# Kernel tuning notes

Hardware: AMD Instinct MI355X
Metric: run time of the kernel (lower is better)

Reference implementation:

```python
import jax, jax.numpy as jnp
import numpy as np

N_NODES = 10000
N_EDGES = 160000
C = 128           # channel multiplicity
D_DOWN = 64       # node_feats_down '64x0e'
D_RAD = 8         # radial basis size
AVG_NEIGH = 16.0
INV_SQRT3 = 1.0 / np.sqrt(3.0)  # CG coeff for 1o x 1o -> 0e


def setup_inputs() -> dict:
    key = jax.random.key(0)
    ks = jax.random.split(key, 20)
    inp = {
        "node_attrs": jax.random.normal(ks[0], (N_NODES, 10), jnp.float32),
        "node_feats": jax.random.normal(ks[1], (N_NODES, 4 * C), jnp.float32),
        "edge_attrs": jax.random.normal(ks[2], (N_EDGES, 4), jnp.float32),
        "edge_feats": jax.random.uniform(ks[3], (N_EDGES, D_RAD), jnp.float32),
        "edge_index": jax.random.randint(ks[4], (N_EDGES, 2), 0, N_NODES, jnp.int32),
        # linear_up: 128x0e+128x1o -> 128x0e+128x1o (per-irrep channel mixing)
        "W_up0": jax.random.normal(ks[5], (C, C), jnp.float32),
        "W_up1": jax.random.normal(ks[6], (C, C), jnp.float32),
        # linear_down: 128x0e+128x1o -> 64x0e (only scalars map)
        "W_down": jax.random.normal(ks[7], (C, D_DOWN), jnp.float32),
        # radial MLP [136, 256, 256, 256, 512]
        "Wm0": jax.random.normal(ks[8], (D_RAD + 2 * D_DOWN, 256), jnp.float32),
        "Wm1": jax.random.normal(ks[9], (256, 256), jnp.float32),
        "Wm2": jax.random.normal(ks[10], (256, 256), jnp.float32),
        "Wm3": jax.random.normal(ks[11], (256, 4 * C), jnp.float32),
        # linear: irreps_mid (2x128x0e + 2x128x1o) -> 128x0e+128x1o
        "W_lin0": jax.random.normal(ks[12], (2 * C, C), jnp.float32),
        "W_lin1": jax.random.normal(ks[13], (2 * C, C), jnp.float32),
        # skip_linear: 128x0e+128x1o -> 128x0e+128x1o
        "W_skip0": jax.random.normal(ks[14], (C, C), jnp.float32),
        "W_skip1": jax.random.normal(ks[15], (C, C), jnp.float32),
    }
    return inp


def _split(x):
    # [N, 512] -> scalars [N,128], vectors [N,128,3]
    return x[:, :C], x[:, C:].reshape(-1, C, 3)


def _irrep_linear(s, v, W0, W1):
    # e3nn Linear with 1/sqrt(fan_in) normalization, per-irrep
    a = (s @ W0) / np.sqrt(C)
    b = jnp.einsum("nic,ij->njc", v, W1) / np.sqrt(C)
    return a, b


def reference(node_attrs, node_feats, edge_attrs, edge_feats, edge_index,
              W_up0, W_up1, W_down, Wm0, Wm1, Wm2, Wm3,
              W_lin0, W_lin1, W_skip0, W_skip1):
    n_nodes = node_feats.shape[0]
    sender = edge_index[:, 0]
    receiver = edge_index[:, 1]

    s, v = _split(node_feats)

    # skip connection
    sc_s, sc_v = _irrep_linear(s, v, W_skip0, W_skip1)
    sc = jnp.concatenate([sc_s, sc_v.reshape(n_nodes, 3 * C)], axis=-1)

    # linear_up / linear_down
    up_s, up_v = _irrep_linear(s, v, W_up0, W_up1)
    down = (s @ W_down) / np.sqrt(C)  # [N, 64]

    # radial MLP on augmented edge feats
    aug = jnp.concatenate([edge_feats, down[sender], down[receiver]], axis=-1)  # [E,136]
    h = jax.nn.silu((aug @ Wm0) / np.sqrt(aug.shape[-1]))
    h = jax.nn.silu((h @ Wm1) / np.sqrt(256.0))
    h = jax.nn.silu((h @ Wm2) / np.sqrt(256.0))
    tpw = (h @ Wm3) / np.sqrt(256.0)  # [E, 512]
    w1, w2, w3, w4 = tpw[:, :C], tpw[:, C:2*C], tpw[:, 2*C:3*C], tpw[:, 3*C:]

    # per-edge CG tensor product (uvu, external weights)
    xs = up_s[sender]           # [E,128] gathered 0e
    xv = up_v[sender]           # [E,128,3] gathered 1o
    y0 = edge_attrs[:, :1]      # [E,1]   sh 0e
    yv = edge_attrs[:, 1:4]     # [E,3]   sh 1o

    out0a = w1 * xs * y0                                       # 0e x 0e -> 0e
    out0b = w4 * jnp.einsum("eic,ec->ei", xv, yv) * INV_SQRT3  # 1o x 1o -> 0e
    out1a = (w2 * xs)[:, :, None] * yv[:, None, :]             # 0e x 1o -> 1o
    out1b = w3[:, :, None] * xv * y0[:, :, None]               # 1o x 0e -> 1o

    mid0 = jnp.concatenate([out0a, out0b], axis=-1)  # [E,256]
    mid1 = jnp.concatenate([out1a, out1b], axis=1)   # [E,256,3]

    # scatter-sum messages to receivers
    m0 = jax.ops.segment_sum(mid0, receiver, num_segments=n_nodes)
    m1 = jax.ops.segment_sum(mid1, receiver, num_segments=n_nodes)

    # final per-irrep linear, divided by avg_num_neighbors
    msg_s = (m0 @ W_lin0) / np.sqrt(2.0 * C) / AVG_NEIGH                       # [N,128]
    msg_v = jnp.einsum("nic,ij->njc", m1, W_lin1) / np.sqrt(2.0 * C) / AVG_NEIGH  # [N,128,3]

    # reshape_irreps: [N, channels, 1+3]
    out = jnp.concatenate([msg_s[:, :, None], msg_v], axis=-1)  # [N,128,4]
    return out, sc
```

## Files before the change

kernel.cpp:

```cpp
#include <hip/hip_runtime.h>
#include <cmath>

#define NN 10000
#define NE 160000
#define INV_SQRT_C 0.08838834764831845f
#define INV_SQRT3F 0.5773502691896258f

typedef _Float16 f16x8 __attribute__((ext_vector_type(8)));
typedef _Float16 f16x4 __attribute__((ext_vector_type(4)));
typedef _Float16 f16x2 __attribute__((ext_vector_type(2)));
typedef float    f32x4 __attribute__((ext_vector_type(4)));

__device__ __forceinline__ float silu_f(float x) {
  return x / (1.f + __expf(-x));
}

__device__ __forceinline__ void wconv_one(
    const float* __restrict__ src, _Float16* __restrict__ dst,
    int Korig, int Kpad, int N, float scale, int P) {
  int total = Kpad * N;
  for (int t = blockIdx.x * blockDim.x + threadIdx.x; t < total;
       t += gridDim.x * blockDim.x) {
    int n = t % N;
    int k = t / N;
    int kb = k >> 5, kk = k & 31;
    int sub = n & (P - 1);
    int n_l = (n & ~(P - 1)) | ((sub & 15) * (P >> 4) + (sub >> 4));
    float v = (k < Korig) ? src[(size_t)k * N + n_l] * scale : 0.f;
    dst[((size_t)(kb * N + n) << 5) + kk] = (_Float16)v;
  }
}

__global__ __launch_bounds__(256) void wconv6(
    const float* __restrict__ s0, const float* __restrict__ s1,
    const float* __restrict__ s2, const float* __restrict__ s3,
    const float* __restrict__ s4, const float* __restrict__ s5,
    _Float16* __restrict__ d0, _Float16* __restrict__ d1,
    _Float16* __restrict__ d2, _Float16* __restrict__ d3,
    _Float16* __restrict__ d4, _Float16* __restrict__ d5) {
  switch (blockIdx.y) {
    case 0: wconv_one(s0, d0, 136, 160, 256, 0.08574929257125442f, 64); break;
    case 1: wconv_one(s1, d1, 256, 256, 256, 0.0625f, 64); break;
    case 2: wconv_one(s2, d2, 256, 256, 256, 0.0625f, 64); break;
    case 3: wconv_one(s3, d3, 256, 256, 512, 0.0625f, 32); break;
    case 4: wconv_one(s4, d4, 256, 256, 128, 1.0f / 256.0f, 32); break;
    default: wconv_one(s5, d5, 256, 256, 128, 1.0f / 256.0f, 32); break;
  }
}

__global__ __launch_bounds__(256) void node_pre_all(
    const float* __restrict__ feats,
    const float* __restrict__ W_up0, const float* __restrict__ W_skip0,
    const float* __restrict__ W_down,
    const float* __restrict__ W_up1, const float* __restrict__ W_skip1,
    _Float16* __restrict__ UPH, _Float16* __restrict__ DOWNH,
    float* __restrict__ out_sc) {
  __shared__ float ls[16 * 384];
  const int t = threadIdx.x;
  if (blockIdx.x < 625) {
    const int n0 = blockIdx.x * 16;
    for (int f = t; f < 16 * 128; f += 256) {
      int r = f >> 7, c = f & 127;
      ls[r * 128 + c] = feats[(size_t)(n0 + r) * 512 + c];
    }
    __syncthreads();
    {
      int j = t & 127, g = t >> 7;
      float au[8] = {0, 0, 0, 0, 0, 0, 0, 0};
      float ak[8] = {0, 0, 0, 0, 0, 0, 0, 0};
      for (int i = 0; i < 128; ++i) {
        float wu = W_up0[(size_t)i * 128 + j];
        float wk = W_skip0[(size_t)i * 128 + j];
#pragma unroll
        for (int r = 0; r < 8; ++r) {
          float s = ls[(g * 8 + r) * 128 + i];
          au[r] += s * wu;
          ak[r] += s * wk;
        }
      }
#pragma unroll
      for (int r = 0; r < 8; ++r) {
        int n = n0 + g * 8 + r;
        UPH[(size_t)n * 512 + j] = (_Float16)(au[r] * INV_SQRT_C);
        out_sc[(size_t)n * 512 + j] = ak[r] * INV_SQRT_C;
      }
    }
    {
      int j = t & 63, g = t >> 6;
      float ad[4] = {0, 0, 0, 0};
      for (int i = 0; i < 128; ++i) {
        float wd = W_down[(size_t)i * 64 + j];
#pragma unroll
        for (int r = 0; r < 4; ++r) ad[r] += ls[(g * 4 + r) * 128 + i] * wd;
      }
#pragma unroll
      for (int r = 0; r < 4; ++r)
        DOWNH[(size_t)(n0 + g * 4 + r) * 64 + j] = (_Float16)(ad[r] * INV_SQRT_C);
    }
  } else {
    const int n0 = (blockIdx.x - 625) * 16;
    for (int f = t; f < 16 * 384; f += 256) {
      int r = f / 384, c = f % 384;
      ls[r * 384 + c] = feats[(size_t)(n0 + r) * 512 + 128 + c];
    }
    __syncthreads();
    int j = t & 127, g = t >> 7;
    float au[8][3], ak[8][3];
#pragma unroll
    for (int r = 0; r < 8; ++r)
#pragma unroll
      for (int c = 0; c < 3; ++c) { au[r][c] = 0.f; ak[r][c] = 0.f; }
    for (int i = 0; i < 128; ++i) {
      float wu = W_up1[(size_t)i * 128 + j];
      float wk = W_skip1[(size_t)i * 128 + j];
#pragma unroll
      for (int r = 0; r < 8; ++r) {
#pragma unroll
        for (int c = 0; c < 3; ++c) {
          float v = ls[(g * 8 + r) * 384 + i * 3 + c];
          au[r][c] += v * wu;
          ak[r][c] += v * wk;
        }
      }
    }
#pragma unroll
    for (int r = 0; r < 8; ++r) {
      int n = n0 + g * 8 + r;
#pragma unroll
      for (int c = 0; c < 3; ++c) {
        UPH[(size_t)n * 512 + 128 + j * 3 + c] = (_Float16)(au[r][c] * INV_SQRT_C);
        out_sc[(size_t)n * 512 + 128 + j * 3 + c] = ak[r][c] * INV_SQRT_C;
      }
    }
  }
}

__global__ void k_count2(const int* __restrict__ edge_index,
                         int* __restrict__ CNT, int* __restrict__ CNT2) {
  int e = blockIdx.x * blockDim.x + threadIdx.x;
  if (e < NE) {
    int2 sr = *(const int2*)&edge_index[(size_t)e * 2];
    atomicAdd(&CNT[sr.y], 1);
    atomicAdd(&CNT2[sr.x], 1);
  }
}

__device__ __forceinline__ void scan_one(const int* __restrict__ CNT,
                                         int* __restrict__ OFF,
                                         int* __restrict__ CUR, int* ts) {
  const int t = threadIdx.x;
  const int base = t * 10;
  int loc[10];
  int s = 0;
#pragma unroll
  for (int i = 0; i < 10; ++i) {
    int idx = base + i;
    int v = (idx < NN) ? CNT[idx] : 0;
    loc[i] = s;
    s += v;
  }
  ts[t] = s;
  __syncthreads();
  for (int off = 1; off < 1024; off <<= 1) {
    int v = (t >= off) ? ts[t - off] : 0;
    __syncthreads();
    ts[t] += v;
    __syncthreads();
  }
  int tp = (t > 0) ? ts[t - 1] : 0;
#pragma unroll
  for (int i = 0; i < 10; ++i) {
    int idx = base + i;
    if (idx < NN) {
      OFF[idx] = tp + loc[i];
      CUR[idx] = tp + loc[i];
    }
  }
  if (t == 1023) OFF[NN] = ts[1023];
}

__global__ __launch_bounds__(1024) void k_scan2(
    const int* __restrict__ CNT, int* __restrict__ OFF, int* __restrict__ CUR,
    const int* __restrict__ CNT2, int* __restrict__ OFF2, int* __restrict__ CUR2) {
  __shared__ int ts[1024];
  if (blockIdx.x == 0) scan_one(CNT, OFF, CUR, ts);
  else                 scan_one(CNT2, OFF2, CUR2, ts);
}

__global__ void k_fill2(const int* __restrict__ edge_index,
                        int* __restrict__ CUR, int* __restrict__ EIDX,
                        int* __restrict__ CUR2, int* __restrict__ SIDX) {
  int e = blockIdx.x * blockDim.x + threadIdx.x;
  if (e < NE) {
    int2 sr = *(const int2*)&edge_index[(size_t)e * 2];
    int ps = atomicAdd(&CUR2[sr.x], 1);
    SIDX[ps] = e;
    int pr = atomicAdd(&CUR[sr.y], 1);
    EIDX[pr] = ps;
  }
}

__device__ __forceinline__ void mlp_layer_256(
    const _Float16* In, _Float16* Out, const _Float16* __restrict__ Wz,
    int m, int g, int wv) {
  f32x4 acc[4][4];
  f32x4 zero4 = {0.f, 0.f, 0.f, 0.f};
#pragma unroll
  for (int rt = 0; rt < 4; ++rt)
#pragma unroll
    for (int ct = 0; ct < 4; ++ct) acc[rt][ct] = zero4;

#pragma unroll
  for (int kb = 0; kb < 8; ++kb) {
    f16x8 a[4], b[4];
#pragma unroll
    for (int rt = 0; rt < 4; ++rt) {
      int row = rt * 16 + m;
      a[rt] = *(const f16x8*)&In[row * 256 + (((kb * 2 + (g >> 1)) ^ m) << 4) + (g & 1) * 8];
    }
#pragma unroll
    for (int ct = 0; ct < 4; ++ct)
      b[ct] = *(const f16x8*)&Wz[((size_t)(kb * 256 + wv * 64 + ct * 16 + m) << 5) + g * 8];
#pragma unroll
    for (int rt = 0; rt < 4; ++rt)
#pragma unroll
      for (int ct = 0; ct < 4; ++ct)
        acc[rt][ct] = __builtin_amdgcn_mfma_f32_16x16x32_f16(a[rt], b[ct], acc[rt][ct], 0, 0, 0);
  }
#pragma unroll
  for (int rt = 0; rt < 4; ++rt)
#pragma unroll
    for (int q = 0; q < 4; ++q) {
      int row = rt * 16 + g * 4 + q;
      f16x4 pk;
#pragma unroll
      for (int ct = 0; ct < 4; ++ct) pk[ct] = (_Float16)silu_f(acc[rt][ct][q]);
      int blk = (wv * 4 + (m >> 2)) ^ (row & 15);
      *(f16x4*)&Out[row * 256 + (blk << 4) + (m & 3) * 4] = pk;
    }
}

__global__ __launch_bounds__(256, 2) void edge_mlp(
    const float* __restrict__ edge_attrs,
    const float* __restrict__ edge_feats,
    const int* __restrict__ edge_index,
    const int* __restrict__ SIDX,
    const _Float16* __restrict__ DOWNH,
    const _Float16* __restrict__ UPH,
    const _Float16* __restrict__ W0h, const _Float16* __restrict__ W1h,
    const _Float16* __restrict__ W2h, const _Float16* __restrict__ W3h,
    const _Float16* __restrict__ WL0h, const _Float16* __restrict__ WL1h,
    _Float16* __restrict__ MIDs) {
  __shared__ _Float16 HA[64 * 256];
  __shared__ _Float16 HB[64 * 256];

  const int tid = threadIdx.x;
  const int lane = tid & 63;
  const int wv = tid >> 6;
  const int m = lane & 15;
  const int g = lane >> 4;
  const int e0 = blockIdx.x * 64;
  const int nw = wv * 64;

  int el_r[4], snd_r[4], rcv_r[4];
#pragma unroll
  for (int rt = 0; rt < 4; ++rt) {
    el_r[rt] = SIDX[e0 + rt * 16 + m];
    int2 sr = *(const int2*)&edge_index[(size_t)el_r[rt] * 2];
    snd_r[rt] = sr.x;
    rcv_r[rt] = sr.y;
  }

  f32x4 zero4 = {0.f, 0.f, 0.f, 0.f};
  f16x8 zf = {0, 0, 0, 0, 0, 0, 0, 0};

  {
    f32x4 acc[4][4];
#pragma unroll
    for (int rt = 0; rt < 4; ++rt)
#pragma unroll
      for (int ct = 0; ct < 4; ++ct) acc[rt][ct] = zero4;

#pragma unroll
    for (int kb = 0; kb < 5; ++kb) {
      const int k0 = kb * 32 + g * 8;
      f16x8 a[4], b[4];
#pragma unroll
      for (int rt = 0; rt < 4; ++rt) {
        if (k0 == 0) {
          const float* ef = &edge_feats[(size_t)el_r[rt] * 8];
          float4 f0 = *(const float4*)ef;
          float4 f1 = *(const float4*)(ef + 4);
          f16x8 av;
          av[0] = (_Float16)f0.x; av[1] = (_Float16)f0.y;
          av[2] = (_Float16)f0.z; av[3] = (_Float16)f0.w;
          av[4] = (_Float16)f1.x; av[5] = (_Float16)f1.y;
          av[6] = (_Float16)f1.z; av[7] = (_Float16)f1.w;
          a[rt] = av;
        } else if (k0 < 72) {
          a[rt] = *(const f16x8*)&DOWNH[(size_t)snd_r[rt] * 64 + (k0 - 8)];
        } else if (k0 < 136) {
          a[rt] = *(const f16x8*)&DOWNH[(size_t)rcv_r[rt] * 64 + (k0 - 72)];
        } else {
          a[rt] = zf;
        }
      }
#pragma unroll
      for (int ct = 0; ct < 4; ++ct)
        b[ct] = *(const f16x8*)&W0h[((size_t)(kb * 256 + nw + ct * 16 + m) << 5) + g * 8];
#pragma unroll
      for (int rt = 0; rt < 4; ++rt)
#pragma unroll
        for (int ct = 0; ct < 4; ++ct)
          acc[rt][ct] = __builtin_amdgcn_mfma_f32_16x16x32_f16(a[rt], b[ct], acc[rt][ct], 0, 0, 0);
    }
#pragma unroll
    for (int rt = 0; rt < 4; ++rt)
#pragma unroll
      for (int q = 0; q < 4; ++q) {
        int row = rt * 16 + g * 4 + q;
        f16x4 pk;
#pragma unroll
        for (int ct = 0; ct < 4; ++ct) pk[ct] = (_Float16)silu_f(acc[rt][ct][q]);
        int blk = (wv * 4 + (m >> 2)) ^ (row & 15);
        *(f16x4*)&HA[row * 256 + (blk << 4) + (m & 3) * 4] = pk;
      }
  }
  __syncthreads();

  mlp_layer_256(HA, HB, W1h, m, g, wv);
  __syncthreads();
  mlp_layer_256(HB, HA, W2h, m, g, wv);
  __syncthreads();

  _Float16* SW = HB;
  _Float16* SP = HB + 64 * 128;

  const int e_loc = lane;
  const int ers = (e_loc ^ (e_loc >> 3)) & 7;
  const int elc = SIDX[e0 + e_loc];
  const int snd_e = edge_index[(size_t)elc * 2];
  const _Float16* uprow = &UPH[(size_t)snd_e * 512];

  auto qgemm = [&](int qbase, f32x4 (&accq)[4][2]) {
#pragma unroll
    for (int rt = 0; rt < 4; ++rt)
#pragma unroll
      for (int ct = 0; ct < 2; ++ct) accq[rt][ct] = zero4;
#pragma unroll
    for (int kb = 0; kb < 8; ++kb) {
      f16x8 a[4], b[2];
#pragma unroll
      for (int rt = 0; rt < 4; ++rt) {
        int row = rt * 16 + m;
        a[rt] = *(const f16x8*)&HA[row * 256 + (((kb * 2 + (g >> 1)) ^ m) << 4) + (g & 1) * 8];
      }
#pragma unroll
      for (int ct = 0; ct < 2; ++ct)
        b[ct] = *(const f16x8*)&W3h[((size_t)(kb * 512 + qbase + wv * 32 + ct * 16 + m) << 5) + g * 8];
#pragma unroll
      for (int rt = 0; rt < 4; ++rt)
#pragma unroll
        for (int ct = 0; ct < 2; ++ct)
          accq[rt][ct] = __builtin_amdgcn_mfma_f32_16x16x32_f16(a[rt], b[ct], accq[rt][ct], 0, 0, 0);
    }
  };

  auto sw_write = [&](const f32x4 (&accq)[4][2]) {
#pragma unroll
    for (int rt = 0; rt < 4; ++rt)
#pragma unroll
      for (int r4 = 0; r4 < 4; ++r4) {
        int row = rt * 16 + g * 4 + r4;
        int rs = (row ^ (row >> 3)) & 7;
        f16x2 pk;
        pk[0] = (_Float16)accq[rt][0][r4];
        pk[1] = (_Float16)accq[rt][1][r4];
        int blk = ((wv * 2 + (m >> 3)) ^ rs) & 7;
        *(f16x2*)&SW[row * 128 + (blk << 4) + (m & 7) * 2] = pk;
      }
  };

  auto fold = [&](const _Float16* __restrict__ WLh, int qpart, f32x4 (&P)[4][2]) {
#pragma unroll
    for (int rt = 0; rt < 4; ++rt)
#pragma unroll
      for (int ct = 0; ct < 2; ++ct) P[rt][ct] = zero4;
#pragma unroll
    for (int kb = 0; kb < 4; ++kb) {
      f16x8 a[4], b[2];
#pragma unroll
      for (int rt = 0; rt < 4; ++rt) {
        int row = rt * 16 + m;
        int rs = (row ^ (row >> 3)) & 7;
        a[rt] = *(const f16x8*)&SP[row * 128 + ((((kb * 2 + (g >> 1)) ^ rs) & 7) << 4) + (g & 1) * 8];
      }
#pragma unroll
      for (int ct = 0; ct < 2; ++ct)
        b[ct] = *(const f16x8*)&WLh[((size_t)((qpart * 4 + kb) * 128 + wv * 32 + ct * 16 + m) << 5) + g * 8];
#pragma unroll
      for (int rt = 0; rt < 4; ++rt)
#pragma unroll
        for (int ct = 0; ct < 2; ++ct)
          P[rt][ct] = __builtin_amdgcn_mfma_f32_16x16x32_f16(a[rt], b[ct], P[rt][ct], 0, 0, 0);
    }
  };

  auto tp_xs = [&]() {
#pragma unroll
    for (int cch = 0; cch < 4; ++cch) {
      int ib = nw / 2 + cch * 8;
      int blk = ((ib >> 4) ^ ers) & 7;
      int off = e_loc * 128 + (blk << 4) + (ib & 15);
      f16x8 swv = *(const f16x8*)&SW[off];
      f16x8 upv = *(const f16x8*)&uprow[ib];
      f16x8 pr = swv * upv;
      *(f16x8*)&SP[off] = pr;
    }
  };

  _Float16 xvb[96];
  auto load_xv = [&]() {
#pragma unroll
    for (int u = 0; u < 12; ++u) {
      f16x8 t = *(const f16x8*)&uprow[128 + wv * 96 + u * 8];
#pragma unroll
      for (int z = 0; z < 8; ++z) xvb[u * 8 + z] = t[z];
    }
  };

  auto tp_w4 = [&]() {
    float4 ea = *(const float4*)&edge_attrs[(size_t)elc * 4];
#pragma unroll
    for (int cch = 0; cch < 4; ++cch) {
      int ib = nw / 2 + cch * 8;
      int blk = ((ib >> 4) ^ ers) & 7;
      int off = e_loc * 128 + (blk << 4) + (ib & 15);
      f16x8 swv = *(const f16x8*)&SW[off];
      f16x8 outv;
#pragma unroll
      for (int z = 0; z < 8; ++z) {
        int k = cch * 8 + z;
        float d = (float)xvb[k * 3] * ea.y + (float)xvb[k * 3 + 1] * ea.z +
                  (float)xvb[k * 3 + 2] * ea.w;
        outv[z] = (_Float16)((float)swv[z] * d);
      }
      *(f16x8*)&SP[off] = outv;
    }
  };

  auto tp_w3 = [&](int c) {
#pragma unroll
    for (int cch = 0; cch < 4; ++cch) {
      int ib = nw / 2 + cch * 8;
      int blk = ((ib >> 4) ^ ers) & 7;
      int off = e_loc * 128 + (blk << 4) + (ib & 15);
      f16x8 swv = *(const f16x8*)&SW[off];
      f16x8 outv;
#pragma unroll
      for (int z = 0; z < 8; ++z) {
        int k = cch * 8 + z;
        outv[z] = swv[z] * xvb[k * 3 + c];
      }
      *(f16x8*)&SP[off] = outv;
    }
  };

  f32x4 accqA[4][2], accqB[4][2];
  f32x4 P1[4][2], P4[4][2], P2[4][2], P3[4][2];

  qgemm(0, accqA);
  sw_write(accqA);
  tp_xs();
  qgemm(384, accqB);
  __syncthreads();
  fold(WL0h, 0, P1);
  sw_write(accqB);
  load_xv();
  __syncthreads();
  tp_w4();
  qgemm(128, accqA);
  __syncthreads();
  fold(WL0h, 1, P4);
  sw_write(accqA);

#pragma unroll
  for (int rt = 0; rt < 4; ++rt)
#pragma unroll
    for (int r4 = 0; r4 < 4; ++r4) {
      int row = rt * 16 + g * 4 + r4;
      int elw = SIDX[e0 + row];
      float4 ea = *(const float4*)&edge_attrs[(size_t)elw * 4];
      f16x2 pk;
      pk[0] = (_Float16)(ea.x * P1[rt][0][r4] + INV_SQRT3F * P4[rt][0][r4]);
      pk[1] = (_Float16)(ea.x * P1[rt][1][r4] + INV_SQRT3F * P4[rt][1][r4]);
      *(f16x2*)&MIDs[(size_t)(e0 + row) * 512 + wv * 32 + m * 2] = pk;
    }
  __syncthreads();
  tp_xs();
  qgemm(256, accqB);
  __syncthreads();
  fold(WL1h, 0, P2);
  sw_write(accqB);
  __syncthreads();

#pragma unroll
  for (int c = 0; c < 3; ++c) {
    tp_w3(c);
    __syncthreads();
    fold(WL1h, 1, P3);
#pragma unroll
    for (int rt = 0; rt < 4; ++rt)
#pragma unroll
      for (int r4 = 0; r4 < 4; ++r4) {
        int row = rt * 16 + g * 4 + r4;
        int elw = SIDX[e0 + row];
        float4 ea = *(const float4*)&edge_attrs[(size_t)elw * 4];
        float yvc = (c == 0) ? ea.y : (c == 1) ? ea.z : ea.w;
        f16x2 pk;
        pk[0] = (_Float16)(yvc * P2[rt][0][r4] + ea.x * P3[rt][0][r4]);
        pk[1] = (_Float16)(yvc * P2[rt][1][r4] + ea.x * P3[rt][1][r4]);
        *(f16x2*)&MIDs[(size_t)(e0 + row) * 512 + 128 + c * 128 + wv * 32 + m * 2] = pk;
      }
    if (c < 2) __syncthreads();
  }
}

__global__ __launch_bounds__(256) void gather_msg(
    const _Float16* __restrict__ MIDs, const int* __restrict__ OFF,
    const int* __restrict__ EIDX, float* __restrict__ out) {
  __shared__ int eb[256];
  __shared__ float os[512];
  const int n = blockIdx.x;
  const int t = threadIdx.x;
  const int beg = OFF[n], end = OFF[n + 1];
  float a0 = 0.f, a1 = 0.f;
  for (int base = beg; base < end; base += 256) {
    int cnt = min(256, end - base);
    __syncthreads();
    if (t < cnt) eb[t] = EIDX[base + t];
    __syncthreads();
    int k = 0;
    for (; k + 4 <= cnt; k += 4) {
      int e0_ = eb[k], e1_ = eb[k + 1], e2_ = eb[k + 2], e3_ = eb[k + 3];
      f16x2 v0 = *(const f16x2*)&MIDs[(size_t)e0_ * 512 + t * 2];
      f16x2 v1 = *(const f16x2*)&MIDs[(size_t)e1_ * 512 + t * 2];
      f16x2 v2 = *(const f16x2*)&MIDs[(size_t)e2_ * 512 + t * 2];
      f16x2 v3 = *(const f16x2*)&MIDs[(size_t)e3_ * 512 + t * 2];
      a0 += (float)v0[0] + (float)v1[0] + (float)v2[0] + (float)v3[0];
      a1 += (float)v0[1] + (float)v1[1] + (float)v2[1] + (float)v3[1];
    }
    for (; k < cnt; ++k) {
      f16x2 v = *(const f16x2*)&MIDs[(size_t)eb[k] * 512 + t * 2];
      a0 += (float)v[0];
      a1 += (float)v[1];
    }
  }
#pragma unroll
  for (int u = 0; u < 2; ++u) {
    int x = t * 2 + u;
    float a = u ? a1 : a0;
    int dst;
    if (x < 128) {
      dst = x * 4;
    } else {
      int xm = x - 128;
      int c = xm >> 7, j = xm & 127;
      dst = j * 4 + 1 + c;
    }
    os[dst] = a;
  }
  __syncthreads();
  *(float2*)&out[(size_t)n * 512 + t * 2] = *(const float2*)&os[t * 2];
}

extern "C" void kernel_launch(void* const* d_in, const int* in_sizes, int n_in,
                              void* d_out, int out_size, void* d_ws, size_t ws_size,
                              hipStream_t stream) {
  const float* node_feats = (const float*)d_in[1];
  const float* edge_attrs = (const float*)d_in[2];
  const float* edge_feats = (const float*)d_in[3];
  const int*   edge_index = (const int*)d_in[4];
  const float* W_up0   = (const float*)d_in[5];
  const float* W_up1   = (const float*)d_in[6];
  const float* W_down  = (const float*)d_in[7];
  const float* Wm0     = (const float*)d_in[8];
  const float* Wm1     = (const float*)d_in[9];
  const float* Wm2     = (const float*)d_in[10];
  const float* Wm3     = (const float*)d_in[11];
  const float* W_lin0  = (const float*)d_in[12];
  const float* W_lin1  = (const float*)d_in[13];
  const float* W_skip0 = (const float*)d_in[14];
  const float* W_skip1 = (const float*)d_in[15];
  float* out = (float*)d_out;

  char* ws = (char*)d_ws;
  size_t off = 0;
  auto alloc = [&](size_t bytes) {
    void* p = ws + off;
    off = (off + bytes + 255) & ~(size_t)255;
    return p;
  };
  _Float16* UPH   = (_Float16*)alloc((size_t)NN * 512 * 2);
  _Float16* DOWNH = (_Float16*)alloc((size_t)NN * 64 * 2);
  _Float16* W0h   = (_Float16*)alloc(160 * 256 * 2);
  _Float16* W1h   = (_Float16*)alloc(256 * 256 * 2);
  _Float16* W2h   = (_Float16*)alloc(256 * 256 * 2);
  _Float16* W3h   = (_Float16*)alloc(256 * 512 * 2);
  _Float16* WL0h  = (_Float16*)alloc(256 * 128 * 2);
  _Float16* WL1h  = (_Float16*)alloc(256 * 128 * 2);
  int*      CNTS  = (int*)alloc((size_t)2 * NN * 4);
  int*      CNT   = CNTS;
  int*      CNT2  = CNTS + NN;
  int*      OFF   = (int*)alloc((size_t)(NN + 1) * 4);
  int*      CUR   = (int*)alloc((size_t)NN * 4);
  int*      EIDX  = (int*)alloc((size_t)NE * 4);
  int*      OFF2  = (int*)alloc((size_t)(NN + 1) * 4);
  int*      CUR2  = (int*)alloc((size_t)NN * 4);
  int*      SIDX  = (int*)alloc((size_t)NE * 4);
  _Float16* MIDs  = (_Float16*)alloc((size_t)NE * 512 * 2);

  hipMemsetAsync(CNTS, 0, (size_t)2 * NN * 4, stream);

  wconv6<<<dim3(128, 6), 256, 0, stream>>>(Wm0, Wm1, Wm2, Wm3, W_lin0, W_lin1,
                                           W0h, W1h, W2h, W3h, WL0h, WL1h);

  node_pre_all<<<1250, 256, 0, stream>>>(node_feats, W_up0, W_skip0, W_down,
                                         W_up1, W_skip1,
                                         UPH, DOWNH, out + (size_t)NN * 512);

  k_count2<<<625, 256, 0, stream>>>(edge_index, CNT, CNT2);
  k_scan2<<<2, 1024, 0, stream>>>(CNT, OFF, CUR, CNT2, OFF2, CUR2);
  k_fill2<<<625, 256, 0, stream>>>(edge_index, CUR, EIDX, CUR2, SIDX);

  edge_mlp<<<2500, 256, 0, stream>>>(edge_attrs, edge_feats, edge_index, SIDX,
                                     DOWNH, UPH, W0h, W1h, W2h, W3h, WL0h, WL1h,
                                     MIDs);
  gather_msg<<<NN, 256, 0, stream>>>(MIDs, OFF, EIDX, out);
}
```

Measured before the change: 474.0 us.

## Merge weight conversion with node precompute and fuse CSR build into cooperative kernel

Weight fp16 conversion and the node linear precompute now run in one kernel launch, using a flat block index to pick the job. The memset, count, scan and fill steps that build the CSR indices are folded into a single cooperative kernel that separates its phases with grid-wide syncs. This cuts the number of kernel launches and the gaps between them, from six plus a memset down to two. In exchange, grid.sync adds barrier cost, and the scan now runs on two 256-thread blocks with a serial 40-element loop per thread, which leaves most of the grid idle during that phase.

```diff
diff --git a/kernel.cpp b/kernel.cpp
--- a/kernel.cpp
+++ b/kernel.cpp
@@ -1,5 +1,8 @@
 #include <hip/hip_runtime.h>
+#include <hip/hip_cooperative_groups.h>
 #include <cmath>
+
+namespace cg = cooperative_groups;
 
 #define NN 10000
 #define NE 160000
@@ -16,11 +19,10 @@
 }
 
 __device__ __forceinline__ void wconv_one(
-    const float* __restrict__ src, _Float16* __restrict__ dst,
+    int bx, const float* __restrict__ src, _Float16* __restrict__ dst,
     int Korig, int Kpad, int N, float scale, int P) {
   int total = Kpad * N;
-  for (int t = blockIdx.x * blockDim.x + threadIdx.x; t < total;
-       t += gridDim.x * blockDim.x) {
+  for (int t = bx * 256 + threadIdx.x; t < total; t += 128 * 256) {
     int n = t % N;
     int k = t / N;
     int kb = k >> 5, kk = k & 31;
@@ -31,24 +33,13 @@
   }
 }
 
-__global__ __launch_bounds__(256) void wconv6(
+__global__ __launch_bounds__(256) void prep(
     const float* __restrict__ s0, const float* __restrict__ s1,
     const float* __restrict__ s2, const float* __restrict__ s3,
     const float* __restrict__ s4, const float* __restrict__ s5,
     _Float16* __restrict__ d0, _Float16* __restrict__ d1,
     _Float16* __restrict__ d2, _Float16* __restrict__ d3,
-    _Float16* __restrict__ d4, _Float16* __restrict__ d5) {
-  switch (blockIdx.y) {
-    case 0: wconv_one(s0, d0, 136, 160, 256, 0.08574929257125442f, 64); break;
-    case 1: wconv_one(s1, d1, 256, 256, 256, 0.0625f, 64); break;
-    case 2: wconv_one(s2, d2, 256, 256, 256, 0.0625f, 64); break;
-    case 3: wconv_one(s3, d3, 256, 256, 512, 0.0625f, 32); break;
-    case 4: wconv_one(s4, d4, 256, 256, 128, 1.0f / 256.0f, 32); break;
-    default: wconv_one(s5, d5, 256, 256, 128, 1.0f / 256.0f, 32); break;
-  }
-}
-
-__global__ __launch_bounds__(256) void node_pre_all(
+    _Float16* __restrict__ d4, _Float16* __restrict__ d5,
     const float* __restrict__ feats,
     const float* __restrict__ W_up0, const float* __restrict__ W_skip0,
     const float* __restrict__ W_down,
@@ -56,9 +47,25 @@
     _Float16* __restrict__ UPH, _Float16* __restrict__ DOWNH,
     float* __restrict__ out_sc) {
   __shared__ float ls[16 * 384];
+  const int b = blockIdx.x;
   const int t = threadIdx.x;
-  if (blockIdx.x < 625) {
-    const int n0 = blockIdx.x * 16;
+
+  if (b < 768) {
+    const int job = b >> 7, bx = b & 127;
+    switch (job) {
+      case 0: wconv_one(bx, s0, d0, 136, 160, 256, 0.08574929257125442f, 64); break;
+      case 1: wconv_one(bx, s1, d1, 256, 256, 256, 0.0625f, 64); break;
+      case 2: wconv_one(bx, s2, d2, 256, 256, 256, 0.0625f, 64); break;
+      case 3: wconv_one(bx, s3, d3, 256, 256, 512, 0.0625f, 32); break;
+      case 4: wconv_one(bx, s4, d4, 256, 256, 128, 1.0f / 256.0f, 32); break;
+      default: wconv_one(bx, s5, d5, 256, 256, 128, 1.0f / 256.0f, 32); break;
+    }
+    return;
+  }
+
+  const int nb = b - 768;
+  if (nb < 625) {
+    const int n0 = nb * 16;
     for (int f = t; f < 16 * 128; f += 256) {
       int r = f >> 7, c = f & 127;
       ls[r * 128 + c] = feats[(size_t)(n0 + r) * 512 + c];
@@ -98,7 +105,7 @@
         DOWNH[(size_t)(n0 + g * 4 + r) * 64 + j] = (_Float16)(ad[r] * INV_SQRT_C);
     }
   } else {
-    const int n0 = (blockIdx.x - 625) * 16;
+    const int n0 = (nb - 625) * 16;
     for (int f = t; f < 16 * 384; f += 256) {
       int r = f / 384, c = f % 384;
       ls[r * 384 + c] = feats[(size_t)(n0 + r) * 512 + 128 + c];
@@ -135,63 +142,60 @@
   }
 }
 
-__global__ void k_count2(const int* __restrict__ edge_index,
-                         int* __restrict__ CNT, int* __restrict__ CNT2) {
-  int e = blockIdx.x * blockDim.x + threadIdx.x;
-  if (e < NE) {
+__global__ __launch_bounds__(256) void k_csr(
+    const int* __restrict__ edge_index,
+    int* CNT, int* CNT2,
+    int* __restrict__ OFF, int* __restrict__ CUR,
+    int* __restrict__ OFF2, int* __restrict__ CUR2,
+    int* __restrict__ EIDX, int* __restrict__ SIDX) {
+  cg::grid_group grid = cg::this_grid();
+  const int t = threadIdx.x;
+  const int gt = blockIdx.x * 256 + t;
+  const int gs = gridDim.x * 256;
+
+  for (int i = gt; i < NN; i += gs) { CNT[i] = 0; CNT2[i] = 0; }
+  grid.sync();
+
+  for (int e = gt; e < NE; e += gs) {
     int2 sr = *(const int2*)&edge_index[(size_t)e * 2];
     atomicAdd(&CNT[sr.y], 1);
     atomicAdd(&CNT2[sr.x], 1);
   }
-}
-
-__device__ __forceinline__ void scan_one(const int* __restrict__ CNT,
-                                         int* __restrict__ OFF,
-                                         int* __restrict__ CUR, int* ts) {
-  const int t = threadIdx.x;
-  const int base = t * 10;
-  int loc[10];
-  int s = 0;
-#pragma unroll
-  for (int i = 0; i < 10; ++i) {
-    int idx = base + i;
-    int v = (idx < NN) ? CNT[idx] : 0;
-    loc[i] = s;
-    s += v;
-  }
-  ts[t] = s;
-  __syncthreads();
-  for (int off = 1; off < 1024; off <<= 1) {
-    int v = (t >= off) ? ts[t - off] : 0;
+  grid.sync();
+
+  if (blockIdx.x < 2) {
+    const int* C = (blockIdx.x == 0) ? CNT : CNT2;
+    int* O = (blockIdx.x == 0) ? OFF : OFF2;
+    int* U = (blockIdx.x == 0) ? CUR : CUR2;
+    __shared__ int ts[256];
+    const int base = t * 40;
+    int s = 0;
+    for (int i = 0; i < 40; ++i) {
+      int idx = base + i;
+      if (idx < NN) s += C[idx];
+    }
+    ts[t] = s;
     __syncthreads();
-    ts[t] += v;
-    __syncthreads();
-  }
-  int tp = (t > 0) ? ts[t - 1] : 0;
-#pragma unroll
-  for (int i = 0; i < 10; ++i) {
-    int idx = base + i;
-    if (idx < NN) {
-      OFF[idx] = tp + loc[i];
-      CUR[idx] = tp + loc[i];
-    }
-  }
-  if (t == 1023) OFF[NN] = ts[1023];
-}
-
-__global__ __launch_bounds__(1024) void k_scan2(
-    const int* __restrict__ CNT, int* __restrict__ OFF, int* __restrict__ CUR,
-    const int* __restrict__ CNT2, int* __restrict__ OFF2, int* __restrict__ CUR2) {
-  __shared__ int ts[1024];
-  if (blockIdx.x == 0) scan_one(CNT, OFF, CUR, ts);
-  else                 scan_one(CNT2, OFF2, CUR2, ts);
-}
-
-__global__ void k_fill2(const int* __restrict__ edge_index,
-                        int* __restrict__ CUR, int* __restrict__ EIDX,
-                        int* __restrict__ CUR2, int* __restrict__ SIDX) {
-  int e = blockIdx.x * blockDim.x + threadIdx.x;
-  if (e < NE) {
+    for (int off = 1; off < 256; off <<= 1) {
+      int v = (t >= off) ? ts[t - off] : 0;
+      __syncthreads();
+      ts[t] += v;
+      __syncthreads();
+    }
+    int run = (t > 0) ? ts[t - 1] : 0;
+    for (int i = 0; i < 40; ++i) {
+      int idx = base + i;
+      if (idx < NN) {
+        O[idx] = run;
+        U[idx] = run;
+        run += C[idx];
+      }
+    }
+    if (t == 255) O[NN] = ts[255];
+  }
+  grid.sync();
+
+  for (int e = gt; e < NE; e += gs) {
     int2 sr = *(const int2*)&edge_index[(size_t)e * 2];
     int ps = atomicAdd(&CUR2[sr.x], 1);
     SIDX[ps] = e;
@@ -609,9 +613,8 @@
   _Float16* W3h   = (_Float16*)alloc(256 * 512 * 2);
   _Float16* WL0h  = (_Float16*)alloc(256 * 128 * 2);
   _Float16* WL1h  = (_Float16*)alloc(256 * 128 * 2);
-  int*      CNTS  = (int*)alloc((size_t)2 * NN * 4);
-  int*      CNT   = CNTS;
-  int*      CNT2  = CNTS + NN;
+  int*      CNT   = (int*)alloc((size_t)NN * 4);
+  int*      CNT2  = (int*)alloc((size_t)NN * 4);
   int*      OFF   = (int*)alloc((size_t)(NN + 1) * 4);
   int*      CUR   = (int*)alloc((size_t)NN * 4);
   int*      EIDX  = (int*)alloc((size_t)NE * 4);
@@ -620,18 +623,20 @@
   int*      SIDX  = (int*)alloc((size_t)NE * 4);
   _Float16* MIDs  = (_Float16*)alloc((size_t)NE * 512 * 2);
 
-  hipMemsetAsync(CNTS, 0, (size_t)2 * NN * 4, stream);
-
-  wconv6<<<dim3(128, 6), 256, 0, stream>>>(Wm0, Wm1, Wm2, Wm3, W_lin0, W_lin1,
-                                           W0h, W1h, W2h, W3h, WL0h, WL1h);
-
-  node_pre_all<<<1250, 256, 0, stream>>>(node_feats, W_up0, W_skip0, W_down,
-                                         W_up1, W_skip1,
-                                         UPH, DOWNH, out + (size_t)NN * 512);
-
-  k_count2<<<625, 256, 0, stream>>>(edge_index, CNT, CNT2);
-  k_scan2<<<2, 1024, 0, stream>>>(CNT, OFF, CUR, CNT2, OFF2, CUR2);
-  k_fill2<<<625, 256, 0, stream>>>(edge_index, CUR, EIDX, CUR2, SIDX);
+  prep<<<2018, 256, 0, stream>>>(Wm0, Wm1, Wm2, Wm3, W_lin0, W_lin1,
+                                 W0h, W1h, W2h, W3h, WL0h, WL1h,
+                                 node_feats, W_up0, W_skip0, W_down,
+                                 W_up1, W_skip1,
+                                 UPH, DOWNH, out + (size_t)NN * 512);
+
+  {
+    const int* ei = edge_index;
+    void* args[] = {(void*)&ei, (void*)&CNT, (void*)&CNT2,
+                    (void*)&OFF, (void*)&CUR, (void*)&OFF2, (void*)&CUR2,
+                    (void*)&EIDX, (void*)&SIDX};
+    hipLaunchCooperativeKernel((const void*)k_csr, dim3(256), dim3(256),
+                               args, 0, stream);
+  }
 
   edge_mlp<<<2500, 256, 0, stream>>>(edge_attrs, edge_feats, edge_index, SIDX,
                                      DOWNH, UPH, W0h, W1h, W2h, W3h, WL0h, WL1h,
```

After: 594.2 us. 1.25x slower.
